# Performance work log

Measured on AMD Instinct MI355X. Metric: run time of the kernel, lower is better.

## Reference

```python
import jax, jax.numpy as jnp
import numpy as np

N_WIRES = 4
N_LAYERS = 2
BSZ = 4096


def _gate(p):
    # combined single-qubit gate RX(p2) @ RZ(p1) @ RY(p0)  (RY applied first)
    a, b, c = p[0] * 0.5, p[1] * 0.5, p[2] * 0.5
    ca, sa = jnp.cos(a), jnp.sin(a)
    ry = jnp.stack([jnp.stack([ca, -sa]), jnp.stack([sa, ca])]).astype(jnp.complex64)
    eb = (jnp.cos(b) - 1j * jnp.sin(b)).astype(jnp.complex64)  # e^{-i b}
    zero = jnp.zeros((), jnp.complex64)
    rz = jnp.stack([jnp.stack([eb, zero]), jnp.stack([zero, jnp.conj(eb)])])
    cc, sc = jnp.cos(c), jnp.sin(c)
    rx = jnp.stack([jnp.stack([cc + 0j, -1j * sc]), jnp.stack([-1j * sc, cc + 0j])]).astype(jnp.complex64)
    return rx @ rz @ ry


def _apply1(state, U, w):
    # state: (N,2,2,2,2); apply 2x2 gate U on wire w
    s = jnp.moveaxis(state, w + 1, 4)
    s = jnp.einsum('nijka,ba->nijkb', s, U)
    return jnp.moveaxis(s, 4, w + 1)


def _cnot(state, c, t):
    s = jnp.moveaxis(state, (c + 1, t + 1), (1, 2))
    s = jnp.stack([s[:, 0], jnp.flip(s[:, 1], axis=1)], axis=1)
    return jnp.moveaxis(s, (1, 2), (c + 1, t + 1))


def _quanv(x, params):
    bsz = x.shape[0]
    # extract 2x2 patches in the same order as the torch loop:
    # [x[r,c], x[r,c+1], x[r+1,c], x[r+1,c+1]], row-major over (r,c)
    p = x.reshape(bsz, 14, 2, 14, 2).transpose(0, 1, 3, 2, 4).reshape(bsz * 196, 4)
    h = p * 0.5
    v = jnp.stack([jnp.cos(h), jnp.sin(h)], axis=-1).astype(jnp.complex64)  # (N,4,2): RY(patch)|0>
    state = jnp.einsum('na,nb,nc,nd->nabcd', v[:, 0], v[:, 1], v[:, 2], v[:, 3])
    for l in range(N_LAYERS):
        for w in range(N_WIRES):
            state = _apply1(state, _gate(params[l, w]), w)
        for w in range(N_WIRES - 1):
            state = _cnot(state, w, w + 1)
        state = _cnot(state, N_WIRES - 1, 0)
    probs = state.real ** 2 + state.imag ** 2  # (N,2,2,2,2)
    z = jnp.array([1.0, -1.0], jnp.float32)
    exps = []
    for w in range(N_WIRES):
        axes = tuple(i for i in range(1, 5) if i != w + 1)
        exps.append(probs.sum(axes) @ z)  # <Z_w>, shape (N,)
    # (N,4) -> (bsz, 196, 4) -> (bsz, 784), patch-major / wire-minor like torch.cat
    return jnp.stack(exps, axis=-1).reshape(bsz, 196 * N_WIRES)


def setup_inputs() -> dict:
    key = jax.random.key(0)
    k1, k2 = jax.random.split(key)
    x = jax.random.uniform(k1, (BSZ, 28, 28), dtype=jnp.float32)
    params = jax.random.normal(k2, (N_LAYERS, N_WIRES, 3), dtype=jnp.float32)
    return {"x": x, "params": params}


def reference(x, params):
    return _quanv(x, params)
```

## Files before the change

### kernel.cpp

```cpp
#include <hip/hip_runtime.h>


typedef _Float16 f16;
typedef _Float16 half8 __attribute__((ext_vector_type(8)));
typedef float f4 __attribute__((ext_vector_type(4)));

#define PK2(a, b) __builtin_bit_cast(float, __builtin_amdgcn_cvt_pkrtz((a), (b)))

__device__ __forceinline__ float2 cmulf(float2 a, float2 b) {
    return make_float2(fmaf(a.x, b.x, -(a.y * b.y)),
                       fmaf(a.x, b.y,   a.y * b.x));
}

__global__ void build_w_kernel(const float* __restrict__ params,
                               f16* __restrict__ wg) {
    __shared__ float4 Gs[8];
    const int t = threadIdx.x;
    if (t < 8) {
        const float* pg = params + t * 3;
        const float ha = 0.5f * pg[0], hb = 0.5f * pg[1], hc = 0.5f * pg[2];
        const float sa = __sinf(ha), ca = __cosf(ha);
        const float sb = __sinf(hb), cb = __cosf(hb);
        const float sc = __sinf(hc), cx = __cosf(hc);
        Gs[t] = make_float4(cx*ca*cb + sc*sa*sb,
                            -(cx*ca*sb + sc*sa*cb),
                            sc*ca*sb - cx*sa*cb,
                            cx*sa*sb - sc*ca*cb);
    }
    __syncthreads();

    const unsigned long long IDX1P = 0x497a2f1c85b6e3d0ULL;
    const unsigned long long INV1P = 0xa3185ce7d46f2b90ULL;
    const int i = t >> 4;
    const int m = t & 15;
    const int jN = (int)((IDX1P >> (i * 4)) & 15);
    float accx = 0.f, accy = 0.f;
    for (int k = 0; k < 16; ++k) {
        const int kN = (int)((INV1P >> (k * 4)) & 15);
        float2 a = make_float2(1.f, 0.f);
        float2 b = make_float2(1.f, 0.f);
#pragma unroll
        for (int w = 0; w < 4; ++w) {
            const float4 g2 = Gs[4 + w];
            const int jb = (jN >> (3 - w)) & 1;
            const int kb = (kN >> (3 - w)) & 1;
            const float ux = jb ? (kb ?  g2.x : -g2.z) : (kb ? g2.z : g2.x);
            const float uy = jb ? (kb ? -g2.y :  g2.w) : (kb ? g2.w : g2.y);
            a = cmulf(a, make_float2(ux, uy));
            const float4 g1 = Gs[w];
            const int kb1 = (k >> (3 - w)) & 1;
            const int mb  = (m >> (3 - w)) & 1;
            const float vx = kb1 ? (mb ?  g1.x : -g1.z) : (mb ? g1.z : g1.x);
            const float vy = kb1 ? (mb ? -g1.y :  g1.w) : (mb ? g1.w : g1.y);
            b = cmulf(b, make_float2(vx, vy));
        }
        const float2 ab = cmulf(a, b);
        accx += ab.x;
        accy += ab.y;
    }
    wg[i * 32 + m]             = (f16)accx;
    wg[i * 32 + 16 + m]        = (f16)0.f;
    wg[(16 + i) * 32 + m]      = (f16)accy;
    wg[(16 + i) * 32 + 16 + m] = (f16)0.f;
}

__global__ __launch_bounds__(256, 6) void quanv_kernel(
        const float* __restrict__ x,
        const f16*   __restrict__ wg,
        float* __restrict__ out)
{
    __shared__ __align__(16) unsigned char SB[4][5120];

    const int t = threadIdx.x;
    const int g = blockIdx.x * 256 + t;
    const int n  = g / 98;
    const int pp = g - n * 98;
    const int r  = pp / 7;
    const int cc = pp - r * 7;

    const float* xb = x + n * 784 + r * 56 + cc * 4;
    const float4 top = *(const float4*)(xb);
    const float4 bot = *(const float4*)(xb + 28);

    const int l   = t & 63;
    const int wid = t >> 6;
    const int q   = l >> 4;
    const int c16 = l & 15;

    const half8 b0 = *(const half8*)(wg + c16 * 32 + q * 8);
    const half8 b1 = *(const half8*)(wg + (16 + c16) * 32 + q * 8);

    const float px[2][4] = {{top.x, top.y, bot.x, bot.y},
                            {top.z, top.w, bot.z, bot.w}};
    float cs[2][4], sn[2][4];
#pragma unroll
    for (int ph = 0; ph < 2; ++ph)
#pragma unroll
        for (int w = 0; w < 4; ++w) {
            const float h = 0.5f * px[ph][w];
            cs[ph][w] = __cosf(h);
            sn[ph][w] = __sinf(h);
        }

    const f4 zf4 = {0.f, 0.f, 0.f, 0.f};
    const float4 zz = make_float4(0.f, 0.f, 0.f, 0.f);
    float4 res[2];

#pragma unroll
    for (int ph = 0; ph < 2; ++ph) {
        const float A0 = cs[ph][0] * cs[ph][1], A1 = cs[ph][0] * sn[ph][1];
        const float A2 = sn[ph][0] * cs[ph][1], A3 = sn[ph][0] * sn[ph][1];
        const float B0 = cs[ph][2] * cs[ph][3], B1 = cs[ph][2] * sn[ph][3];
        const float B2 = sn[ph][2] * cs[ph][3], B3 = sn[ph][2] * sn[ph][3];

        f16* st = (f16*)(SB[wid] + l * 80);
        *(float4*)(st)      = make_float4(PK2(A0*B0, A0*B1), PK2(A0*B2, A0*B3),
                                          PK2(A1*B0, A1*B1), PK2(A1*B2, A1*B3));
        *(float4*)(st + 8)  = make_float4(PK2(A2*B0, A2*B1), PK2(A2*B2, A2*B3),
                                          PK2(A3*B0, A3*B1), PK2(A3*B2, A3*B3));
        *(float4*)(st + 16) = zz;
        *(float4*)(st + 24) = zz;

        f4 d0[4], d1[4];
#pragma unroll
        for (int mm = 0; mm < 4; ++mm) {
            const half8 am = *(const half8*)(SB[wid] + (mm*16 + c16)*80 + q*16);
            d0[mm] = __builtin_amdgcn_mfma_f32_16x16x32_f16(am, b0, zf4, 0, 0, 0);
            d1[mm] = __builtin_amdgcn_mfma_f32_16x16x32_f16(am, b1, zf4, 0, 0, 0);
        }

        float* prb = (float*)SB[wid];
#pragma unroll
        for (int mm = 0; mm < 4; ++mm)
#pragma unroll
            for (int reg = 0; reg < 4; ++reg) {
                const float pv = fmaf(d0[mm][reg], d0[mm][reg],
                                      d1[mm][reg] * d1[mm][reg]);
                prb[(mm*16 + q*4 + reg) * 20 + c16] = pv;
            }

        const float4 p0 = *(const float4*)(prb + l * 20);
        const float4 p1 = *(const float4*)(prb + l * 20 + 4);
        const float4 p2 = *(const float4*)(prb + l * 20 + 8);
        const float4 p3 = *(const float4*)(prb + l * 20 + 12);

        const float t00 = p0.x + p0.y + p0.z + p0.w;
        const float t01 = p1.x + p1.y + p1.z + p1.w;
        const float t10 = p2.x + p2.y + p2.z + p2.w;
        const float t11 = p3.x + p3.y + p3.z + p3.w;
        const float e0 = (t00 + t01) - (t10 + t11);
        const float e1 = (t00 - t01) + (t10 - t11);

        const float u00 = p0.x + p1.x + p2.x + p3.x;
        const float u01 = p0.y + p1.y + p2.y + p3.y;
        const float u10 = p0.z + p1.z + p2.z + p3.z;
        const float u11 = p0.w + p1.w + p2.w + p3.w;
        const float e2 = (u00 + u01) - (u10 + u11);
        const float e3 = (u00 - u01) + (u10 - u11);
        res[ph] = make_float4(e0, e1, e2, e3);
    }

    *(float4*)(out + g * 8)     = res[0];
    *(float4*)(out + g * 8 + 4) = res[1];
}

extern "C" void kernel_launch(void* const* d_in, const int* in_sizes, int n_in,
                              void* d_out, int out_size, void* d_ws, size_t ws_size,
                              hipStream_t stream) {
    const float* x      = (const float*)d_in[0];
    const float* params = (const float*)d_in[1];
    float* out = (float*)d_out;
    f16* wg = (f16*)d_ws;

    build_w_kernel<<<1, 256, 0, stream>>>(params, wg);
    const int npairs = 4096 * 98;
    quanv_kernel<<<npairs / 256, 256, 0, stream>>>(x, wg, out);
}
```

Measured before the change: 71.03 us.

## Fuse circuit-matrix construction into main kernel, rebuilt per block in shared memory

Removes the separate single-block build_w kernel and its launch. Each block of the main kernel now builds the 16x16 complex circuit matrix itself in LDS. The build is split into a per-thread product-of-gates stage and a 16-term matrix multiply, with padded rows for the MFMA operand loads. This drops one kernel launch and the serial dependency between the two kernels. In exchange every block does redundant trig and matmul work and adds two extra __syncthreads plus extra LDS use, which may reduce occupancy.

```diff
diff --git a/kernel.cpp b/kernel.cpp
--- a/kernel.cpp
+++ b/kernel.cpp
@@ -12,10 +12,26 @@
                        fmaf(a.x, b.y,   a.y * b.x));
 }
 
-__global__ void build_w_kernel(const float* __restrict__ params,
-                               f16* __restrict__ wg) {
+__global__ __launch_bounds__(256, 6) void quanv_kernel(
+        const float* __restrict__ x,
+        const float* __restrict__ params,
+        float* __restrict__ out)
+{
     __shared__ float4 Gs[8];
+    __shared__ __align__(16) unsigned char SB[4][5120];
+    __shared__ __align__(16) f16 WG[32 * 40];
+
     const int t = threadIdx.x;
+    const int g = blockIdx.x * 256 + t;
+    const int n  = g / 98;
+    const int pp = g - n * 98;
+    const int r  = pp / 7;
+    const int cc = pp - r * 7;
+
+    const float* xb = x + n * 784 + r * 56 + cc * 4;
+    const float4 top = *(const float4*)(xb);
+    const float4 bot = *(const float4*)(xb + 28);
+
     if (t < 8) {
         const float* pg = params + t * 3;
         const float ha = 0.5f * pg[0], hb = 0.5f * pg[1], hc = 0.5f * pg[2];
@@ -29,14 +45,14 @@
     }
     __syncthreads();
 
-    const unsigned long long IDX1P = 0x497a2f1c85b6e3d0ULL;
-    const unsigned long long INV1P = 0xa3185ce7d46f2b90ULL;
-    const int i = t >> 4;
-    const int m = t & 15;
-    const int jN = (int)((IDX1P >> (i * 4)) & 15);
-    float accx = 0.f, accy = 0.f;
-    for (int k = 0; k < 16; ++k) {
-        const int kN = (int)((INV1P >> (k * 4)) & 15);
+    float2* Af = (float2*)(SB[0]);
+    float2* Bf = (float2*)(SB[0] + 2048);
+    {
+        const unsigned long long IDX1P = 0x497a2f1c85b6e3d0ULL;
+        const unsigned long long INV1P = 0xa3185ce7d46f2b90ULL;
+        const int hi = t >> 4, lo = t & 15;
+        const int jN = (int)((IDX1P >> (hi * 4)) & 15);
+        const int kN = (int)((INV1P >> (lo * 4)) & 15);
         float2 a = make_float2(1.f, 0.f);
         float2 b = make_float2(1.f, 0.f);
 #pragma unroll
@@ -48,47 +64,40 @@
             const float uy = jb ? (kb ? -g2.y :  g2.w) : (kb ? g2.w : g2.y);
             a = cmulf(a, make_float2(ux, uy));
             const float4 g1 = Gs[w];
-            const int kb1 = (k >> (3 - w)) & 1;
-            const int mb  = (m >> (3 - w)) & 1;
+            const int kb1 = (hi >> (3 - w)) & 1;
+            const int mb  = (lo >> (3 - w)) & 1;
             const float vx = kb1 ? (mb ?  g1.x : -g1.z) : (mb ? g1.z : g1.x);
             const float vy = kb1 ? (mb ? -g1.y :  g1.w) : (mb ? g1.w : g1.y);
             b = cmulf(b, make_float2(vx, vy));
         }
-        const float2 ab = cmulf(a, b);
-        accx += ab.x;
-        accy += ab.y;
+        Af[hi * 16 + lo] = a;
+        Bf[hi * 16 + lo] = b;
     }
-    wg[i * 32 + m]             = (f16)accx;
-    wg[i * 32 + 16 + m]        = (f16)0.f;
-    wg[(16 + i) * 32 + m]      = (f16)accy;
-    wg[(16 + i) * 32 + 16 + m] = (f16)0.f;
-}
+    __syncthreads();
 
-__global__ __launch_bounds__(256, 6) void quanv_kernel(
-        const float* __restrict__ x,
-        const f16*   __restrict__ wg,
-        float* __restrict__ out)
-{
-    __shared__ __align__(16) unsigned char SB[4][5120];
-
-    const int t = threadIdx.x;
-    const int g = blockIdx.x * 256 + t;
-    const int n  = g / 98;
-    const int pp = g - n * 98;
-    const int r  = pp / 7;
-    const int cc = pp - r * 7;
-
-    const float* xb = x + n * 784 + r * 56 + cc * 4;
-    const float4 top = *(const float4*)(xb);
-    const float4 bot = *(const float4*)(xb + 28);
+    {
+        const int i = t >> 4, m = t & 15;
+        float accx = 0.f, accy = 0.f;
+#pragma unroll
+        for (int k = 0; k < 16; ++k) {
+            const float2 ab = cmulf(Af[i * 16 + k], Bf[k * 16 + m]);
+            accx += ab.x;
+            accy += ab.y;
+        }
+        WG[i * 40 + m]              = (f16)accx;
+        WG[i * 40 + 16 + m]         = (f16)0.f;
+        WG[(16 + i) * 40 + m]       = (f16)accy;
+        WG[(16 + i) * 40 + 16 + m]  = (f16)0.f;
+    }
+    __syncthreads();
 
     const int l   = t & 63;
     const int wid = t >> 6;
     const int q   = l >> 4;
     const int c16 = l & 15;
 
-    const half8 b0 = *(const half8*)(wg + c16 * 32 + q * 8);
-    const half8 b1 = *(const half8*)(wg + (16 + c16) * 32 + q * 8);
+    const half8 b0 = *(const half8*)&WG[c16 * 40 + q * 8];
+    const half8 b1 = *(const half8*)&WG[(16 + c16) * 40 + q * 8];
 
     const float px[2][4] = {{top.x, top.y, bot.x, bot.y},
                             {top.z, top.w, bot.z, bot.w}};
@@ -170,9 +179,7 @@
     const float* x      = (const float*)d_in[0];
     const float* params = (const float*)d_in[1];
     float* out = (float*)d_out;
-    f16* wg = (f16*)d_ws;
 
-    build_w_kernel<<<1, 256, 0, stream>>>(params, wg);
     const int npairs = 4096 * 98;
-    quanv_kernel<<<npairs / 256, 256, 0, stream>>>(x, wg, out);
+    quanv_kernel<<<npairs / 256, 256, 0, stream>>>(x, params, out);
 }
```

After: 70.04 us. About the same (-1.4%).
